# Optimization experiments

Hardware: AMD Instinct MI355X
Metric: run time of the kernel (lower is better)

The kernel has to match this reference:

```python
import jax, jax.numpy as jnp
import numpy as np

H = 8
SPLIT = 1
# deterministic stand-in for random.shuffle(range(8)) in the original
_PERM = np.random.RandomState(0).permutation(H)
SERIES_IDX = jnp.asarray(_PERM[SPLIT:])  # 7 heads
CROSS_IDX = jnp.asarray(_PERM[:SPLIT])   # 1 head


def setup_inputs() -> dict:
    key = jax.random.key(0)
    ks = jax.random.split(key, 5)
    B, L, E = 8, 1024, 64
    shp = (B, L, H, E)
    return {
        "queries": jax.random.normal(ks[0], shp, dtype=jnp.float32),
        "keys": jax.random.normal(ks[1], shp, dtype=jnp.float32),
        "keysT": jax.random.normal(ks[2], shp, dtype=jnp.float32),
        "values": jax.random.normal(ks[3], shp, dtype=jnp.float32),
        "valuesT": jax.random.normal(ks[4], shp, dtype=jnp.float32),
    }


def reference(queries, keys, keysT, values, valuesT):
    B, L, _, E = queries.shape
    scale = 1.0 / jnp.sqrt(jnp.asarray(E, dtype=queries.dtype))
    neg_inf = jnp.asarray(-jnp.inf, dtype=queries.dtype)

    # head split (gather along head dim)
    sq = queries[:, :, SERIES_IDX]   # [B,L,7,E]
    sk = keys[:, :, SERIES_IDX]      # [B,S,7,E]
    sv = values[:, :, SERIES_IDX]    # [B,S,7,D]
    cq = queries[:, :, CROSS_IDX]    # [B,L,1,E]
    ckT = keysT[:, :, CROSS_IDX]     # [B,C,1,E]
    cvT = valuesT[:, :, CROSS_IDX]   # [B,C,1,D]

    # causal mask: True above the diagonal -> disallowed
    causal = jnp.triu(jnp.ones((L, L), dtype=bool), k=1)  # [L,L]

    # series branch
    scores = jnp.einsum('blne,bsne->bnls', sq, sk)  # [B,7,L,S]
    scores = jnp.where(causal[None, None], neg_inf, scores * scale)
    series = jax.nn.softmax(scores, axis=-1)
    V = jnp.einsum('bhls,bshd->blhd', series, sv)   # [B,L,7,D]

    # cross branch
    cscores = jnp.einsum('blme,bcme->bmlc', cq, ckT)  # [B,1,L,C]
    cscores = jnp.where(causal[None, None], neg_inf, cscores * scale)
    crosses = jax.nn.softmax(cscores, axis=-1)
    V_cross = jnp.einsum('bhlc,bchd->blhd', crosses, cvT)  # [B,L,1,D]

    return jnp.concatenate([V, V_cross], axis=2)  # [B,L,8,D]
```

## Files before the change

kernel.cpp:

```cpp
#include <hip/hip_runtime.h>
#include <math.h>

#define Lq 1024
#define Hq 8
#define Eq 64
#define LDW 72

#define SRC_HEAD_PACKED 0x64503712u

typedef __bf16 bf16_t;
typedef __bf16 bf16x8 __attribute__((ext_vector_type(8)));
typedef __bf16 bf16x4 __attribute__((ext_vector_type(4)));
typedef float floatx4 __attribute__((ext_vector_type(4)));

__device__ __forceinline__ bf16x8 cvt8(const float4 a, const float4 b) {
    bf16x8 r;
    r[0] = (bf16_t)a.x; r[1] = (bf16_t)a.y; r[2] = (bf16_t)a.z; r[3] = (bf16_t)a.w;
    r[4] = (bf16_t)b.x; r[5] = (bf16_t)b.y; r[6] = (bf16_t)b.z; r[7] = (bf16_t)b.w;
    return r;
}

__global__ __launch_bounds__(256, 2)
void attn_mfma(const float* __restrict__ Q, const float* __restrict__ Ks,
               const float* __restrict__ KTs, const float* __restrict__ Vs,
               const float* __restrict__ VTs, float* __restrict__ out) {
    const int p    = blockIdx.x;
    const int slot = blockIdx.y;
    const int b    = blockIdx.z;
    const int h    = (SRC_HEAD_PACKED >> (slot * 4)) & 0xF;
    const float* __restrict__ Kp = (slot == 7) ? KTs : Ks;
    const float* __restrict__ Vp = (slot == 7) ? VTs : Vs;
    const int pA = p, pB = 15 - p;

    const int tid  = threadIdx.x;
    const int wv   = tid >> 6;
    const int lane = tid & 63;
    const int ln16 = lane & 15;
    const int quad = lane >> 4;

    __shared__ alignas(16) unsigned short k_lds[2][64][LDW];
    __shared__ alignas(16) unsigned short vt_lds[2][64][LDW];
    __shared__ alignas(16) unsigned short ptA[4][16][LDW];
    __shared__ alignas(16) unsigned short ptB[4][16][LDW];

    const float qs = 0.125f * 1.44269504f;
    bf16x8 qfA[2], qfB[2];
    {
        const int rA = pA * 64 + wv * 16 + ln16;
        const int rB = pB * 64 + wv * 16 + ln16;
        const float* qa = Q + (((size_t)b * Lq + rA) * Hq + h) * Eq + quad * 8;
        const float* qb = Q + (((size_t)b * Lq + rB) * Hq + h) * Eq + quad * 8;
        #pragma unroll
        for (int ec = 0; ec < 2; ++ec) {
            float4 f0 = ((const float4*)(qa + ec * 32))[0];
            float4 f1 = ((const float4*)(qa + ec * 32))[1];
            float4 g0 = ((const float4*)(qb + ec * 32))[0];
            float4 g1 = ((const float4*)(qb + ec * 32))[1];
            f0.x*=qs; f0.y*=qs; f0.z*=qs; f0.w*=qs; f1.x*=qs; f1.y*=qs; f1.z*=qs; f1.w*=qs;
            g0.x*=qs; g0.y*=qs; g0.z*=qs; g0.w*=qs; g1.x*=qs; g1.y*=qs; g1.z*=qs; g1.w*=qs;
            qfA[ec] = cvt8(f0, f1);
            qfB[ec] = cvt8(g0, g1);
        }
    }

    floatx4 OA[4], OB[4];
    #pragma unroll
    for (int i = 0; i < 4; ++i) { OA[i] = (floatx4){0,0,0,0}; OB[i] = (floatx4){0,0,0,0}; }
    float mA = -INFINITY, lA = 0.f, mB = -INFINITY, lB = 0.f;

    const int kj = tid >> 2;
    const int kc = ((((tid & 3) + (tid >> 2)) & 3)) * 16;
    const int vd = lane;
    const int vk = (((tid >> 6) + (lane >> 4)) & 3) * 16;

    float4 kq[4];
    float  vq[16];
    auto load_tile = [&](int kt) {
        const float* kb = Kp + (((size_t)b * Lq + kt * 64 + kj) * Hq + h) * Eq + kc;
        kq[0] = ((const float4*)kb)[0]; kq[1] = ((const float4*)kb)[1];
        kq[2] = ((const float4*)kb)[2]; kq[3] = ((const float4*)kb)[3];
        const float* vb = Vp + (((size_t)b * Lq + kt * 64 + vk) * Hq + h) * Eq + vd;
        #pragma unroll
        for (int i = 0; i < 16; ++i) vq[i] = vb[(size_t)i * (Hq * Eq)];
    };
    auto stage = [&](int buf) {
        *(bf16x8*)&k_lds[buf][kj][kc]     = cvt8(kq[0], kq[1]);
        *(bf16x8*)&k_lds[buf][kj][kc + 8] = cvt8(kq[2], kq[3]);
        const float4* vq4 = (const float4*)vq;
        *(bf16x8*)&vt_lds[buf][vd][vk]     = cvt8(vq4[0], vq4[1]);
        *(bf16x8*)&vt_lds[buf][vd][vk + 8] = cvt8(vq4[2], vq4[3]);
    };

    auto process = [&](const bf16x8 (&qf)[2], bf16x8 (&kf)[4][2], bf16x8 (&vf)[4][2],
                       floatx4 (&O)[4], float& m, float& l, bool diag,
                       unsigned short (*ptw)[LDW]) {
        floatx4 s[4];
        #pragma unroll
        for (int nc = 0; nc < 4; ++nc) {
            floatx4 acc = (floatx4){0,0,0,0};
            acc = __builtin_amdgcn_mfma_f32_16x16x32_bf16(kf[nc][0], qf[0], acc, 0, 0, 0);
            acc = __builtin_amdgcn_mfma_f32_16x16x32_bf16(kf[nc][1], qf[1], acc, 0, 0, 0);
            s[nc] = acc;
        }
        if (diag) {
            const int rin = wv * 16 + ln16;
            #pragma unroll
            for (int nc = 0; nc < 4; ++nc)
                #pragma unroll
                for (int r = 0; r < 4; ++r)
                    if (nc * 16 + quad * 4 + r > rin) s[nc][r] = -INFINITY;
        }
        float mn = s[0][0];
        #pragma unroll
        for (int nc = 0; nc < 4; ++nc)
            #pragma unroll
            for (int r = 0; r < 4; ++r) mn = fmaxf(mn, s[nc][r]);
        mn = fmaxf(mn, __shfl_xor(mn, 16, 64));
        mn = fmaxf(mn, __shfl_xor(mn, 32, 64));
        mn = fmaxf(mn, m);
        const float alpha = __builtin_amdgcn_exp2f(m - mn);
        m = mn;
        float ps = 0.f;
        float pv[4][4];
        #pragma unroll
        for (int nc = 0; nc < 4; ++nc)
            #pragma unroll
            for (int r = 0; r < 4; ++r) { pv[nc][r] = __builtin_amdgcn_exp2f(s[nc][r] - mn); ps += pv[nc][r]; }
        ps += __shfl_xor(ps, 16, 64);
        ps += __shfl_xor(ps, 32, 64);
        l = l * alpha + ps;
        #pragma unroll
        for (int dc = 0; dc < 4; ++dc) O[dc] *= alpha;
        #pragma unroll
        for (int nc = 0; nc < 4; ++nc) {
            bf16x4 pk;
            pk[0] = (bf16_t)pv[nc][0]; pk[1] = (bf16_t)pv[nc][1];
            pk[2] = (bf16_t)pv[nc][2]; pk[3] = (bf16_t)pv[nc][3];
            *(bf16x4*)&ptw[ln16][nc * 16 + quad * 4] = pk;
        }
        bf16x8 pf0 = *(const bf16x8*)&ptw[ln16][quad * 8];
        bf16x8 pf1 = *(const bf16x8*)&ptw[ln16][32 + quad * 8];
        #pragma unroll
        for (int dc = 0; dc < 4; ++dc) {
            O[dc] = __builtin_amdgcn_mfma_f32_16x16x32_bf16(vf[dc][0], pf0, O[dc], 0, 0, 0);
            O[dc] = __builtin_amdgcn_mfma_f32_16x16x32_bf16(vf[dc][1], pf1, O[dc], 0, 0, 0);
        }
    };

    load_tile(0);
    stage(0);
    if (pB >= 1) load_tile(1);
    __syncthreads();

    for (int kt = 0; kt <= pB; ++kt) {
        const int cur = kt & 1, nxt = cur ^ 1;
        bf16x8 kf[4][2], vf[4][2];
        #pragma unroll
        for (int c = 0; c < 4; ++c) {
            kf[c][0] = *(const bf16x8*)&k_lds[cur][c * 16 + ln16][quad * 8];
            kf[c][1] = *(const bf16x8*)&k_lds[cur][c * 16 + ln16][32 + quad * 8];
            vf[c][0] = *(const bf16x8*)&vt_lds[cur][c * 16 + ln16][quad * 8];
            vf[c][1] = *(const bf16x8*)&vt_lds[cur][c * 16 + ln16][32 + quad * 8];
        }
        if (kt + 1 <= pB) stage(nxt);
        if (kt + 2 <= pB) load_tile(kt + 2);
        if (kt <= pA) process(qfA, kf, vf, OA, mA, lA, kt == pA, ptA[wv]);
        process(qfB, kf, vf, OB, mB, lB, kt == pB, ptB[wv]);
        if (kt < pB) __syncthreads();
    }

    {
        const float inv = 1.0f / lA;
        const int row = pA * 64 + wv * 16 + ln16;
        float* op = out + (((size_t)b * Lq + row) * Hq + slot) * Eq + quad * 4;
        #pragma unroll
        for (int dc = 0; dc < 4; ++dc) {
            float4 o; o.x = OA[dc][0] * inv; o.y = OA[dc][1] * inv;
            o.z = OA[dc][2] * inv; o.w = OA[dc][3] * inv;
            *(float4*)(op + dc * 16) = o;
        }
    }
    {
        const float inv = 1.0f / lB;
        const int row = pB * 64 + wv * 16 + ln16;
        float* op = out + (((size_t)b * Lq + row) * Hq + slot) * Eq + quad * 4;
        #pragma unroll
        for (int dc = 0; dc < 4; ++dc) {
            float4 o; o.x = OB[dc][0] * inv; o.y = OB[dc][1] * inv;
            o.z = OB[dc][2] * inv; o.w = OB[dc][3] * inv;
            *(float4*)(op + dc * 16) = o;
        }
    }
}

extern "C" void kernel_launch(void* const* d_in, const int* in_sizes, int n_in,
                              void* d_out, int out_size, void* d_ws, size_t ws_size,
                              hipStream_t stream) {
    const float* queries = (const float*)d_in[0];
    const float* keys    = (const float*)d_in[1];
    const float* keysT   = (const float*)d_in[2];
    const float* values  = (const float*)d_in[3];
    const float* valuesT = (const float*)d_in[4];
    float* out = (float*)d_out;

    dim3 grid(8, Hq, 8);
    dim3 block(256);
    attn_mfma<<<grid, block, 0, stream>>>(queries, keys, keysT, values, valuesT, out);
}
```

Baseline: 145.7 us.

## Feed P directly from registers into PV MFMA, drop LDS transpose

Removes the per-wave LDS round trip used to transpose the softmax probabilities. The P tile is now fed straight from registers as the A operand of 16x16x16 bf16 MFMAs, with O laid out transposed, so the per-row rescale and final normalization need lane shuffles and the output stores become scalar. The LDS stage and prefetch are also moved ahead of the fragment reads. In exchange it issues twice as many smaller MFMAs, adds more LDS reads for V fragments, and stores output less efficiently.

After: 147.1 us. Within noise of the previous version (+1.0%).

```diff
diff --git a/kernel.cpp b/kernel.cpp
--- a/kernel.cpp
+++ b/kernel.cpp
@@ -10,8 +10,8 @@
 
 typedef __bf16 bf16_t;
 typedef __bf16 bf16x8 __attribute__((ext_vector_type(8)));
-typedef __bf16 bf16x4 __attribute__((ext_vector_type(4)));
-typedef float floatx4 __attribute__((ext_vector_type(4)));
+typedef short  shortx4 __attribute__((ext_vector_type(4)));
+typedef float  floatx4 __attribute__((ext_vector_type(4)));
 
 __device__ __forceinline__ bf16x8 cvt8(const float4 a, const float4 b) {
     bf16x8 r;
@@ -40,8 +40,6 @@
 
     __shared__ alignas(16) unsigned short k_lds[2][64][LDW];
     __shared__ alignas(16) unsigned short vt_lds[2][64][LDW];
-    __shared__ alignas(16) unsigned short ptA[4][16][LDW];
-    __shared__ alignas(16) unsigned short ptB[4][16][LDW];
 
     const float qs = 0.125f * 1.44269504f;
     bf16x8 qfA[2], qfB[2];
@@ -69,9 +67,9 @@
     float mA = -INFINITY, lA = 0.f, mB = -INFINITY, lB = 0.f;
 
     const int kj = tid >> 2;
-    const int kc = ((((tid & 3) + (tid >> 2)) & 3)) * 16;
+    const int kc = ((((tid & 3) + kj) & 3)) * 16;
     const int vd = lane;
-    const int vk = (((tid >> 6) + (lane >> 4)) & 3) * 16;
+    const int vk = (((tid >> 6) + (vd >> 4)) & 3) * 16;
 
     float4 kq[4];
     float  vq[16];
@@ -91,9 +89,8 @@
         *(bf16x8*)&vt_lds[buf][vd][vk + 8] = cvt8(vq4[2], vq4[3]);
     };
 
-    auto process = [&](const bf16x8 (&qf)[2], bf16x8 (&kf)[4][2], bf16x8 (&vf)[4][2],
-                       floatx4 (&O)[4], float& m, float& l, bool diag,
-                       unsigned short (*ptw)[LDW]) {
+    auto process = [&](const bf16x8 (&qf)[2], bf16x8 (&kf)[4][2], shortx4 (&vf)[4][4],
+                       floatx4 (&O)[4], float& m, float& l, bool diag) {
         floatx4 s[4];
         #pragma unroll
         for (int nc = 0; nc < 4; ++nc) {
@@ -129,22 +126,26 @@
         ps += __shfl_xor(ps, 16, 64);
         ps += __shfl_xor(ps, 32, 64);
         l = l * alpha + ps;
-        #pragma unroll
-        for (int dc = 0; dc < 4; ++dc) O[dc] *= alpha;
+        float aO[4];
+        #pragma unroll
+        for (int r = 0; r < 4; ++r) aO[r] = __shfl(alpha, quad * 4 + r, 64);
+        #pragma unroll
+        for (int dc = 0; dc < 4; ++dc)
+            #pragma unroll
+            for (int r = 0; r < 4; ++r) O[dc][r] *= aO[r];
+        shortx4 pa[4];
         #pragma unroll
         for (int nc = 0; nc < 4; ++nc) {
-            bf16x4 pk;
-            pk[0] = (bf16_t)pv[nc][0]; pk[1] = (bf16_t)pv[nc][1];
-            pk[2] = (bf16_t)pv[nc][2]; pk[3] = (bf16_t)pv[nc][3];
-            *(bf16x4*)&ptw[ln16][nc * 16 + quad * 4] = pk;
-        }
-        bf16x8 pf0 = *(const bf16x8*)&ptw[ln16][quad * 8];
-        bf16x8 pf1 = *(const bf16x8*)&ptw[ln16][32 + quad * 8];
-        #pragma unroll
-        for (int dc = 0; dc < 4; ++dc) {
-            O[dc] = __builtin_amdgcn_mfma_f32_16x16x32_bf16(vf[dc][0], pf0, O[dc], 0, 0, 0);
-            O[dc] = __builtin_amdgcn_mfma_f32_16x16x32_bf16(vf[dc][1], pf1, O[dc], 0, 0, 0);
-        }
+            union { shortx4 s4; bf16_t bf[4]; } u;
+            u.bf[0] = (bf16_t)pv[nc][0]; u.bf[1] = (bf16_t)pv[nc][1];
+            u.bf[2] = (bf16_t)pv[nc][2]; u.bf[3] = (bf16_t)pv[nc][3];
+            pa[nc] = u.s4;
+        }
+        #pragma unroll
+        for (int dc = 0; dc < 4; ++dc)
+            #pragma unroll
+            for (int nc = 0; nc < 4; ++nc)
+                O[dc] = __builtin_amdgcn_mfma_f32_16x16x16bf16_1k(pa[nc], vf[dc][nc], O[dc], 0, 0, 0);
     };
 
     load_tile(0);
@@ -154,41 +155,49 @@
 
     for (int kt = 0; kt <= pB; ++kt) {
         const int cur = kt & 1, nxt = cur ^ 1;
-        bf16x8 kf[4][2], vf[4][2];
+        if (kt + 1 <= pB) stage(nxt);
+        if (kt + 2 <= pB) load_tile(kt + 2);
+        bf16x8 kf[4][2];
+        shortx4 vf[4][4];
         #pragma unroll
         for (int c = 0; c < 4; ++c) {
             kf[c][0] = *(const bf16x8*)&k_lds[cur][c * 16 + ln16][quad * 8];
             kf[c][1] = *(const bf16x8*)&k_lds[cur][c * 16 + ln16][32 + quad * 8];
-            vf[c][0] = *(const bf16x8*)&vt_lds[cur][c * 16 + ln16][quad * 8];
-            vf[c][1] = *(const bf16x8*)&vt_lds[cur][c * 16 + ln16][32 + quad * 8];
-        }
-        if (kt + 1 <= pB) stage(nxt);
-        if (kt + 2 <= pB) load_tile(kt + 2);
-        if (kt <= pA) process(qfA, kf, vf, OA, mA, lA, kt == pA, ptA[wv]);
-        process(qfB, kf, vf, OB, mB, lB, kt == pB, ptB[wv]);
+        }
+        #pragma unroll
+        for (int dc = 0; dc < 4; ++dc)
+            #pragma unroll
+            for (int nc = 0; nc < 4; ++nc)
+                vf[dc][nc] = *(const shortx4*)&vt_lds[cur][dc * 16 + ln16][nc * 16 + quad * 4];
+        if (kt <= pA) process(qfA, kf, vf, OA, mA, lA, kt == pA);
+        process(qfB, kf, vf, OB, mB, lB, kt == pB);
         if (kt < pB) __syncthreads();
     }
 
     {
-        const float inv = 1.0f / lA;
-        const int row = pA * 64 + wv * 16 + ln16;
-        float* op = out + (((size_t)b * Lq + row) * Hq + slot) * Eq + quad * 4;
-        #pragma unroll
-        for (int dc = 0; dc < 4; ++dc) {
-            float4 o; o.x = OA[dc][0] * inv; o.y = OA[dc][1] * inv;
-            o.z = OA[dc][2] * inv; o.w = OA[dc][3] * inv;
-            *(float4*)(op + dc * 16) = o;
+        float lo[4];
+        #pragma unroll
+        for (int r = 0; r < 4; ++r) lo[r] = __shfl(lA, quad * 4 + r, 64);
+        const int rowb = pA * 64 + wv * 16 + quad * 4;
+        #pragma unroll
+        for (int r = 0; r < 4; ++r) {
+            const float inv = 1.0f / lo[r];
+            float* op = out + (((size_t)b * Lq + rowb + r) * Hq + slot) * Eq + ln16;
+            #pragma unroll
+            for (int dc = 0; dc < 4; ++dc) op[dc * 16] = OA[dc][r] * inv;
         }
     }
     {
-        const float inv = 1.0f / lB;
-        const int row = pB * 64 + wv * 16 + ln16;
-        float* op = out + (((size_t)b * Lq + row) * Hq + slot) * Eq + quad * 4;
-        #pragma unroll
-        for (int dc = 0; dc < 4; ++dc) {
-            float4 o; o.x = OB[dc][0] * inv; o.y = OB[dc][1] * inv;
-            o.z = OB[dc][2] * inv; o.w = OB[dc][3] * inv;
-            *(float4*)(op + dc * 16) = o;
+        float lo[4];
+        #pragma unroll
+        for (int r = 0; r < 4; ++r) lo[r] = __shfl(lB, quad * 4 + r, 64);
+        const int rowb = pB * 64 + wv * 16 + quad * 4;
+        #pragma unroll
+        for (int r = 0; r < 4; ++r) {
+            const float inv = 1.0f / lo[r];
+            float* op = out + (((size_t)b * Lq + rowb + r) * Hq + slot) * Eq + ln16;
+            #pragma unroll
+            for (int dc = 0; dc < 4; ++dc) op[dc * 16] = OB[dc][r] * inv;
         }
     }
 }
```
